# Optimization experiments

Hardware: AMD Instinct MI355X
Metric: run time of the kernel (lower is better)

## Reference

```python
import jax, jax.numpy as jnp
import numpy as np

C, H, W = 64, 32, 32  # feature planes are (1, 64, 32, 32)
M = 1_048_576         # number of query points


def bilinear_sample(plane, coords):
    """torch.nn.functional.grid_sample, mode='bilinear', padding_mode='zeros',
    align_corners=True, for a single plane.
    plane: (C, H, W); coords: (M, 2) with (x, y) in [-1, 1] convention.
    Returns (M, C)."""
    c, h, w = plane.shape
    # align_corners=True mapping: -1 -> 0, +1 -> size-1
    x = (coords[:, 0] + 1.0) * 0.5 * (w - 1)
    y = (coords[:, 1] + 1.0) * 0.5 * (h - 1)
    x0 = jnp.floor(x)
    y0 = jnp.floor(y)
    wx1 = x - x0
    wy1 = y - y0
    wx0 = 1.0 - wx1
    wy0 = 1.0 - wy1

    def gather(xi, yi):
        xi = xi.astype(jnp.int32)
        yi = yi.astype(jnp.int32)
        valid = (xi >= 0) & (xi < w) & (yi >= 0) & (yi < h)  # zeros padding
        xc = jnp.clip(xi, 0, w - 1)
        yc = jnp.clip(yi, 0, h - 1)
        v = plane[:, yc, xc]  # (C, M)
        return jnp.where(valid[None, :], v, 0.0)

    out = (gather(x0, y0) * (wx0 * wy0)[None, :]
           + gather(x0 + 1, y0) * (wx1 * wy0)[None, :]
           + gather(x0, y0 + 1) * (wx0 * wy1)[None, :]
           + gather(x0 + 1, y0 + 1) * (wx1 * wy1)[None, :])
    return out.T  # (M, C)


def setup_inputs() -> dict:
    key = jax.random.key(0)
    ks = jax.random.split(key, 10)
    coordinates = jax.random.normal(ks[0], (1, M, 3), dtype=jnp.float32)
    # tri-plane embeddings: randn * 0.1, shape (1, C, H, W)
    plane_xy = jax.random.normal(ks[1], (1, C, H, W), dtype=jnp.float32) * 0.1
    plane_yz = jax.random.normal(ks[2], (1, C, H, W), dtype=jnp.float32) * 0.1
    plane_xz = jax.random.normal(ks[3], (1, C, H, W), dtype=jnp.float32) * 0.1
    # MLP 64 -> 128 -> 128 -> 1 (torch Linear weight shape = (out, in))
    # layer 0: first_layer_sine_init -> U(-1/64, 1/64)
    w1 = jax.random.uniform(ks[4], (128, 64), jnp.float32, -1.0 / 64, 1.0 / 64)
    b1 = jnp.zeros((128,), jnp.float32)
    # layers 1,2: frequency_init(30) -> U(-sqrt(6/in)/30, sqrt(6/in)/30)
    s2 = np.sqrt(6.0 / 128) / 30.0
    w2 = jax.random.uniform(ks[5], (128, 128), jnp.float32, -s2, s2)
    b2 = jnp.zeros((128,), jnp.float32)
    w3 = jax.random.uniform(ks[6], (1, 128), jnp.float32, -s2, s2)
    b3 = jnp.zeros((1,), jnp.float32)
    return {"coordinates": coordinates, "plane_xy": plane_xy, "plane_yz": plane_yz,
            "plane_xz": plane_xz, "w1": w1, "b1": b1, "w2": w2, "b2": b2,
            "w3": w3, "b3": b3}


def reference(coordinates, plane_xy, plane_yz, plane_xz, w1, b1, w2, b2, w3, b3):
    # coordinates: (1, M, 3); planes have leading batch dim of 1 (torch requires
    # grid batch == plane batch, so batch_size is structurally 1).
    samp = jax.vmap(bilinear_sample, in_axes=(None, 0))
    xy = samp(plane_xy[0], coordinates[..., 0:2])   # (1, M, C)
    yz = samp(plane_yz[0], coordinates[..., 1:3])   # (1, M, C)
    xz = samp(plane_xz[0], coordinates[..., ::2])   # (1, M, C)
    features = xy * yz * xz                          # aggregate_fn='prod'
    h = jax.nn.relu(jnp.einsum('bmc,oc->bmo', features, w1) + b1)
    h = jax.nn.relu(jnp.einsum('bmc,oc->bmo', h, w2) + b2)
    out = jnp.einsum('bmc,oc->bmo', h, w3) + b3      # (1, M, 1)
    return out
```

## Files before the change

### kernel.cpp

```cpp
#include <hip/hip_runtime.h>

#define MPTS 1048576

typedef _Float16 f16;
typedef _Float16 f16x4 __attribute__((ext_vector_type(4)));
typedef _Float16 f16x8 __attribute__((ext_vector_type(8)));
typedef float f32x4 __attribute__((ext_vector_type(4)));

static const size_t OFF_Z    = 0;
static const size_t OFF_CNT  = 64;
static const size_t OFF_PL   = 256;
static const size_t OFF_W1H  = OFF_PL + 786432;
static const size_t OFF_W2H  = OFF_W1H + 16384;
static const size_t OFF_BCNT = OFF_W2H + 32768;
static const size_t OFF_BOFF = OFF_BCNT + 4096;
static const size_t OFF_LIST = OFF_BOFF + 4096;
static const size_t OFF_PC   = OFF_LIST + (size_t)MPTS*4;
static const size_t WS_LIST  = OFF_PC;
static const size_t WS_PC    = OFF_PC + (size_t)MPTS*16;

__device__ __forceinline__ int iclamp(int v, int lo, int hi) {
    return v < lo ? lo : (v > hi ? hi : v);
}
__device__ __forceinline__ int imin(int a, int b) { return a < b ? a : b; }

__device__ __forceinline__ bool isact(float x, float y, float z) {
    float px = fmaf(x, 15.5f, 15.5f);
    float py = fmaf(y, 15.5f, 15.5f);
    float pz = fmaf(z, 15.5f, 15.5f);
    return (px > -1.0f) & (px < 32.0f) & (py > -1.0f) & (py < 32.0f) &
           (pz > -1.0f) & (pz < 32.0f);
}

struct Bi { int o00, o01, o10, o11; float w00, w01, w10, w11; };

__device__ __forceinline__ Bi mkbi(float pa, float pb) {
    float fa = floorf(pa), fb = floorf(pb);
    int ia0 = (int)fa, ib0 = (int)fb;
    int ia1 = ia0 + 1, ib1 = ib0 + 1;
    float wa1 = pa - fa, wa0 = 1.0f - wa1;
    float wb1 = pb - fb, wb0 = 1.0f - wb1;
    float va0 = (ia0 >= 0 && ia0 < 32) ? wa0 : 0.0f;
    float va1 = (ia1 >= 0 && ia1 < 32) ? wa1 : 0.0f;
    float vb0 = (ib0 >= 0 && ib0 < 32) ? wb0 : 0.0f;
    float vb1 = (ib1 >= 0 && ib1 < 32) ? wb1 : 0.0f;
    int ca0 = iclamp(ia0, 0, 31), ca1 = iclamp(ia1, 0, 31);
    int cb0 = iclamp(ib0, 0, 31), cb1 = iclamp(ib1, 0, 31);
    Bi r;
    r.o00 = (cb0 * 32 + ca0) * 64; r.o01 = (cb0 * 32 + ca1) * 64;
    r.o10 = (cb1 * 32 + ca0) * 64; r.o11 = (cb1 * 32 + ca1) * 64;
    r.w00 = va0 * vb0; r.w01 = va1 * vb0; r.w10 = va0 * vb1; r.w11 = va1 * vb1;
    return r;
}

__device__ __forceinline__ float4 bsamp4(const float* __restrict__ base, const Bi B) {
    float4 g00 = *(const float4*)(base + B.o00);
    float4 g01 = *(const float4*)(base + B.o01);
    float4 g10 = *(const float4*)(base + B.o10);
    float4 g11 = *(const float4*)(base + B.o11);
    float4 r;
    r.x = fmaf(B.w00, g00.x, fmaf(B.w01, g01.x, fmaf(B.w10, g10.x, B.w11 * g11.x)));
    r.y = fmaf(B.w00, g00.y, fmaf(B.w01, g01.y, fmaf(B.w10, g10.y, B.w11 * g11.y)));
    r.z = fmaf(B.w00, g00.z, fmaf(B.w01, g01.z, fmaf(B.w10, g10.z, B.w11 * g11.z)));
    r.w = fmaf(B.w00, g00.w, fmaf(B.w01, g01.w, fmaf(B.w10, g10.w, B.w11 * g11.w)));
    return r;
}

__device__ __forceinline__ void samp16(const float* __restrict__ pl,
                                       float pa, float pb, int c0,
                                       float* __restrict__ f, const bool mult) {
    Bi B = mkbi(pa, pb);
    const float4* p00 = (const float4*)(pl + B.o00 + c0);
    const float4* p01 = (const float4*)(pl + B.o01 + c0);
    const float4* p10 = (const float4*)(pl + B.o10 + c0);
    const float4* p11 = (const float4*)(pl + B.o11 + c0);
#pragma unroll
    for (int q = 0; q < 4; ++q) {
        float4 g00 = p00[q], g01 = p01[q], g10 = p10[q], g11 = p11[q];
        float vx = fmaf(B.w00, g00.x, fmaf(B.w01, g01.x, fmaf(B.w10, g10.x, B.w11 * g11.x)));
        float vy = fmaf(B.w00, g00.y, fmaf(B.w01, g01.y, fmaf(B.w10, g10.y, B.w11 * g11.y)));
        float vz = fmaf(B.w00, g00.z, fmaf(B.w01, g01.z, fmaf(B.w10, g10.z, B.w11 * g11.z)));
        float vw = fmaf(B.w00, g00.w, fmaf(B.w01, g01.w, fmaf(B.w10, g10.w, B.w11 * g11.w)));
        if (mult) {
            f[4*q+0] *= vx; f[4*q+1] *= vy; f[4*q+2] *= vz; f[4*q+3] *= vw;
        } else {
            f[4*q+0] = vx; f[4*q+1] = vy; f[4*q+2] = vz; f[4*q+3] = vw;
        }
    }
}

__global__ void k_prep(const float* __restrict__ pxy, const float* __restrict__ pyz,
                       const float* __restrict__ pxz,
                       const float* __restrict__ w1, const float* __restrict__ w2,
                       const float* __restrict__ b1, const float* __restrict__ b2,
                       const float* __restrict__ w3, const float* __restrict__ b3,
                       float* __restrict__ planes, f16* __restrict__ w1h,
                       f16* __restrict__ w2h, float* __restrict__ zout) {
    if (blockIdx.x == 864) {
        int p = threadIdx.x;
        if (p >= 128) return;
        float h2p = b2[p];
        for (int o = 0; o < 128; ++o) h2p += w2[p * 128 + o] * fmaxf(b1[o], 0.0f);
        __shared__ float red[128];
        red[p] = fmaxf(h2p, 0.0f) * w3[p];
        __syncthreads();
        for (int s = 64; s > 0; s >>= 1) {
            if (p < s) red[p] += red[p + s];
            __syncthreads();
        }
        if (p == 0) *zout = red[0] + b3[0];
        return;
    }
    int tid = blockIdx.x * 256 + threadIdx.x;
    if (tid < 3 * 65536) {
        int t = tid >> 16;
        int r = tid & 65535;
        int hw = r >> 6;
        int c = r & 63;
        const float* src = (t == 0) ? pxy : ((t == 1) ? pyz : pxz);
        planes[tid] = src[c * 1024 + hw];
    } else if (tid < 3 * 65536 + 8192) {
        int r = tid - 3 * 65536;
        w1h[r] = (f16)w1[r];
    } else {
        int r = tid - (3 * 65536 + 8192);
        w2h[r] = (f16)w2[r];
    }
}

__global__ void k_count(const float* __restrict__ coords, const float* __restrict__ zptr,
                        int* __restrict__ bcnt, float* __restrict__ out) {
    int t = threadIdx.x, bid = blockIdx.x;
    const float4* c4 = (const float4*)coords + 768 * (size_t)bid + 3 * t;
    float4 a = c4[0], b = c4[1], c = c4[2];
    int base = bid * 1024 + t * 4;
    float z = *zptr;
    bool a0 = isact(a.x, a.y, a.z);
    bool a1 = isact(a.w, b.x, b.y);
    bool a2 = isact(b.z, b.w, c.x);
    bool a3 = isact(c.y, c.z, c.w);
    if (!a0) out[base + 0] = z;
    if (!a1) out[base + 1] = z;
    if (!a2) out[base + 2] = z;
    if (!a3) out[base + 3] = z;
    int s = (int)a0 + (int)a1 + (int)a2 + (int)a3;
#pragma unroll
    for (int off = 1; off <= 32; off <<= 1) s += __shfl_xor(s, off, 64);
    __shared__ int wt[4];
    if ((t & 63) == 0) wt[t >> 6] = s;
    __syncthreads();
    if (t == 0) bcnt[bid] = wt[0] + wt[1] + wt[2] + wt[3];
}

__global__ void k_scan(const int* __restrict__ bcnt, int* __restrict__ boff,
                       int* __restrict__ cnt) {
    int t = threadIdx.x, lane = t & 63, wv = t >> 6;
    int mine = bcnt[t];
    int incl = mine;
#pragma unroll
    for (int off = 1; off <= 32; off <<= 1) {
        int v = __shfl_up(incl, off, 64);
        if (lane >= off) incl += v;
    }
    __shared__ int wtot[16];
    if (lane == 63) wtot[wv] = incl;
    __syncthreads();
    int wexcl = 0;
#pragma unroll
    for (int k = 0; k < 16; ++k) wexcl += (k < wv) ? wtot[k] : 0;
    boff[t] = wexcl + incl - mine;
    if (t == 1023) *cnt = wexcl + incl;
}

template<bool PC>
__global__ void k_scatter(const float* __restrict__ coords, const int* __restrict__ boff,
                          int* __restrict__ list, float4* __restrict__ pc4) {
    int t = threadIdx.x, bid = blockIdx.x, lane = t & 63, wv = t >> 6;
    const float4* c4 = (const float4*)coords + 768 * (size_t)bid + 3 * t;
    float4 a = c4[0], b = c4[1], c = c4[2];
    int base = bid * 1024 + t * 4;
    float xs[4] = {a.x, a.w, b.z, c.y};
    float ys[4] = {a.y, b.x, b.w, c.z};
    float zs[4] = {a.z, b.y, c.x, c.w};
    bool act[4];
#pragma unroll
    for (int j = 0; j < 4; ++j) act[j] = isact(xs[j], ys[j], zs[j]);
    int mine = (int)act[0] + (int)act[1] + (int)act[2] + (int)act[3];
    int incl = mine;
#pragma unroll
    for (int off = 1; off <= 32; off <<= 1) {
        int v = __shfl_up(incl, off, 64);
        if (lane >= off) incl += v;
    }
    __shared__ int wtot[4];
    if (lane == 63) wtot[wv] = incl;
    __syncthreads();
    int wexcl = 0;
#pragma unroll
    for (int k = 0; k < 4; ++k) wexcl += (k < wv) ? wtot[k] : 0;
    int pos = boff[bid] + wexcl + incl - mine;
#pragma unroll
    for (int j = 0; j < 4; ++j) {
        if (act[j]) {
            list[pos] = base + j;
            if (PC) {
                float4 p;
                p.x = fmaf(xs[j], 15.5f, 15.5f);
                p.y = fmaf(ys[j], 15.5f, 15.5f);
                p.z = fmaf(zs[j], 15.5f, 15.5f);
                p.w = 0.0f;
                pc4[pos] = p;
            }
            ++pos;
        }
    }
}

__global__ __launch_bounds__(256, 2)
void k_fused(const float4* __restrict__ pc4, const float* __restrict__ planes,
             const f16* __restrict__ w1h, const f16* __restrict__ w2h,
             const float* __restrict__ b1, const float* __restrict__ b2,
             const float* __restrict__ w3, const float* __restrict__ b3,
             const int* __restrict__ cnt, const int* __restrict__ list,
             float* __restrict__ out) {
    const int n = *cnt;
    const int tile = blockIdx.x;
    if (tile * 64 >= n) return;

    __shared__ __attribute__((aligned(16))) f16 Fs[64 * 64];
    __shared__ __attribute__((aligned(16))) f16 H1s[64 * 128];
    __shared__ float outp[4][64];

    const int t   = threadIdx.x;
    const int wv  = t >> 6;
    const int l   = t & 63;
    const int l15 = l & 15;
    const int lg  = l >> 4;
    const int ptw = t >> 4;
    const int cq  = t & 15;

    const float* pl0 = planes;
    const float* pl1 = planes + 65536;
    const float* pl2 = planes + 131072;
    const float b3v = b3[0];

#pragma unroll
    for (int pass = 0; pass < 4; ++pass) {
        int pt = pass * 16 + ptw;
        int ic = imin(tile * 64 + pt, n - 1);
        float4 c = pc4[ic];
        Bi B0 = mkbi(c.x, c.y);
        Bi B1 = mkbi(c.y, c.z);
        Bi B2 = mkbi(c.x, c.z);
        float4 s0 = bsamp4(pl0 + cq * 4, B0);
        float4 s1 = bsamp4(pl1 + cq * 4, B1);
        float4 s2 = bsamp4(pl2 + cq * 4, B2);
        float4 f;
        f.x = (s0.x * s1.x) * s2.x;
        f.y = (s0.y * s1.y) * s2.y;
        f.z = (s0.z * s1.z) * s2.z;
        f.w = (s0.w * s1.w) * s2.w;
        f16x4 pk;
        pk[0] = (f16)f.x; pk[1] = (f16)f.y; pk[2] = (f16)f.z; pk[3] = (f16)f.w;
        *(f16x4*)((char*)Fs + pt * 128 + ((cq * 8) ^ ((pt & 7) << 4))) = pk;
    }
    __syncthreads();

    f16x8 af[4][2];
#pragma unroll
    for (int Mt = 0; Mt < 4; ++Mt) {
        int row = Mt * 16 + l15;
        const char* rb = (const char*)Fs + row * 128;
        int sw = (row & 7) << 4;
        af[Mt][0] = *(const f16x8*)(rb + ((lg * 16) ^ sw));
        af[Mt][1] = *(const f16x8*)(rb + ((64 + lg * 16) ^ sw));
    }

    f16x8 wf1[2][2];
    f16x8 wf2[2][4];
    f32x4 b1q[2], b2q[2], w3q[2];
#pragma unroll
    for (int ntl = 0; ntl < 2; ++ntl) {
        int nrow = (wv * 2 + ntl) * 16 + l15;
        wf1[ntl][0] = *(const f16x8*)(w1h + nrow * 64 + lg * 8);
        wf1[ntl][1] = *(const f16x8*)(w1h + nrow * 64 + 32 + lg * 8);
#pragma unroll
        for (int ks = 0; ks < 4; ++ks)
            wf2[ntl][ks] = *(const f16x8*)(w2h + nrow * 128 + ks * 32 + lg * 8);
        int nb = (wv * 2 + ntl) * 16 + lg * 4;
        b1q[ntl] = *(const f32x4*)(b1 + nb);
        b2q[ntl] = *(const f32x4*)(b2 + nb);
        w3q[ntl] = *(const f32x4*)(w3 + nb);
    }

    f32x4 acc[2][4];
#pragma unroll
    for (int ntl = 0; ntl < 2; ++ntl)
#pragma unroll
        for (int Mt = 0; Mt < 4; ++Mt) acc[ntl][Mt] = b1q[ntl];
#pragma unroll
    for (int Mt = 0; Mt < 4; ++Mt) {
#pragma unroll
        for (int ntl = 0; ntl < 2; ++ntl) {
            acc[ntl][Mt] = __builtin_amdgcn_mfma_f32_16x16x32_f16(wf1[ntl][0], af[Mt][0], acc[ntl][Mt], 0, 0, 0);
            acc[ntl][Mt] = __builtin_amdgcn_mfma_f32_16x16x32_f16(wf1[ntl][1], af[Mt][1], acc[ntl][Mt], 0, 0, 0);
        }
    }

#pragma unroll
    for (int ntl = 0; ntl < 2; ++ntl) {
#pragma unroll
        for (int Mt = 0; Mt < 4; ++Mt) {
            int pt = Mt * 16 + l15;
            int off = (((wv * 2 + ntl) * 32 + lg * 8) ^ ((pt & 7) << 4));
            f16x4 h;
            h[0] = (f16)fmaxf(acc[ntl][Mt][0], 0.0f);
            h[1] = (f16)fmaxf(acc[ntl][Mt][1], 0.0f);
            h[2] = (f16)fmaxf(acc[ntl][Mt][2], 0.0f);
            h[3] = (f16)fmaxf(acc[ntl][Mt][3], 0.0f);
            *(f16x4*)((char*)H1s + pt * 256 + off) = h;
        }
    }
    __syncthreads();

    f32x4 acc2[2][4];
#pragma unroll
    for (int ntl = 0; ntl < 2; ++ntl)
#pragma unroll
        for (int Mt = 0; Mt < 4; ++Mt) acc2[ntl][Mt] = b2q[ntl];
#pragma unroll
    for (int Mt = 0; Mt < 4; ++Mt) {
        int row = Mt * 16 + l15;
        const char* rb = (const char*)H1s + row * 256;
        int sw = (row & 7) << 4;
        f16x8 a0 = *(const f16x8*)(rb + ((lg * 16) ^ sw));
        f16x8 a1 = *(const f16x8*)(rb + ((64 + lg * 16) ^ sw));
        f16x8 a2 = *(const f16x8*)(rb + ((128 + lg * 16) ^ sw));
        f16x8 a3 = *(const f16x8*)(rb + ((192 + lg * 16) ^ sw));
#pragma unroll
        for (int ntl = 0; ntl < 2; ++ntl) {
            acc2[ntl][Mt] = __builtin_amdgcn_mfma_f32_16x16x32_f16(wf2[ntl][0], a0, acc2[ntl][Mt], 0, 0, 0);
            acc2[ntl][Mt] = __builtin_amdgcn_mfma_f32_16x16x32_f16(wf2[ntl][1], a1, acc2[ntl][Mt], 0, 0, 0);
            acc2[ntl][Mt] = __builtin_amdgcn_mfma_f32_16x16x32_f16(wf2[ntl][2], a2, acc2[ntl][Mt], 0, 0, 0);
            acc2[ntl][Mt] = __builtin_amdgcn_mfma_f32_16x16x32_f16(wf2[ntl][3], a3, acc2[ntl][Mt], 0, 0, 0);
        }
    }

#pragma unroll
    for (int Mt = 0; Mt < 4; ++Mt) {
        float s = 0.0f;
#pragma unroll
        for (int ntl = 0; ntl < 2; ++ntl)
#pragma unroll
            for (int r = 0; r < 4; ++r)
                s = fmaf(fmaxf(acc2[ntl][Mt][r], 0.0f), w3q[ntl][r], s);
        s += __shfl_xor(s, 16, 64);
        s += __shfl_xor(s, 32, 64);
        if (lg == 0) outp[wv][Mt * 16 + l15] = s;
    }
    __syncthreads();
    if (t < 64) {
        int gi = tile * 64 + t;
        if (gi < n) {
            float s = outp[0][t] + outp[1][t] + outp[2][t] + outp[3][t] + b3v;
            out[list[gi]] = s;
        }
    }
}

__global__ __launch_bounds__(256, 2)
void k_mlp(const float* __restrict__ coords, const float* __restrict__ planes,
           const f16* __restrict__ w1h, const f16* __restrict__ w2h,
           const float* __restrict__ b1, const float* __restrict__ b2,
           const float* __restrict__ w3, const float* __restrict__ b3,
           const int* __restrict__ cnt, const int* __restrict__ list,
           float* __restrict__ out) {
    const int n = *cnt;
    const int tile = blockIdx.x;
    if (tile * 64 >= n) return;

    __shared__ __attribute__((aligned(16))) f16 Fs[64 * 64];
    __shared__ __attribute__((aligned(16))) f16 H1s[64 * 128];
    __shared__ float outp[4][64];

    const int t   = threadIdx.x;
    const int wv  = t >> 6;
    const int l   = t & 63;
    const int l15 = l & 15;
    const int lg  = l >> 4;

    const float* pl0 = planes;
    const float* pl1 = planes + 65536;
    const float* pl2 = planes + 131072;

    f16x8 wf1[2][2];
    f16x8 wf2[2][4];
    float b1v[2], b2v[2], w3v[2];
#pragma unroll
    for (int ntl = 0; ntl < 2; ++ntl) {
        int nrow = (wv * 2 + ntl) * 16 + l15;
#pragma unroll
        for (int ks = 0; ks < 2; ++ks)
            wf1[ntl][ks] = *(const f16x8*)(w1h + nrow * 64 + ks * 32 + lg * 8);
#pragma unroll
        for (int ks = 0; ks < 4; ++ks)
            wf2[ntl][ks] = *(const f16x8*)(w2h + nrow * 128 + ks * 32 + lg * 8);
        b1v[ntl] = b1[nrow];
        b2v[ntl] = b2[nrow];
        w3v[ntl] = w3[nrow];
    }
    const float b3v = b3[0];

    {
        int pt = t >> 2, c0 = (t & 3) * 16;
        int ic = imin(tile * 64 + pt, n - 1);
        int i = list[ic];
        float px = fmaf(coords[3 * i + 0], 15.5f, 15.5f);
        float py = fmaf(coords[3 * i + 1], 15.5f, 15.5f);
        float pz = fmaf(coords[3 * i + 2], 15.5f, 15.5f);
        float feat[16];
        samp16(pl0, px, py, c0, feat, false);
        samp16(pl1, py, pz, c0, feat, true);
        samp16(pl2, px, pz, c0, feat, true);
        int sw = (pt & 7) << 4;
        char* Fb = (char*)Fs + pt * 128;
        f16x8 pk;
#pragma unroll
        for (int j = 0; j < 8; ++j) pk[j] = (f16)feat[j];
        *(f16x8*)(Fb + ((c0 * 2) ^ sw)) = pk;
#pragma unroll
        for (int j = 0; j < 8; ++j) pk[j] = (f16)feat[8 + j];
        *(f16x8*)(Fb + ((c0 * 2 + 16) ^ sw)) = pk;
    }
    __syncthreads();

    f32x4 acc[2][4];
#pragma unroll
    for (int ntl = 0; ntl < 2; ++ntl) {
        f32x4 ini = {b1v[ntl], b1v[ntl], b1v[ntl], b1v[ntl]};
#pragma unroll
        for (int Mt = 0; Mt < 4; ++Mt) acc[ntl][Mt] = ini;
    }
#pragma unroll
    for (int Mt = 0; Mt < 4; ++Mt) {
        int row = Mt * 16 + l15;
        const char* rb = (const char*)Fs + row * 128;
        int sw = (row & 7) << 4;
        f16x8 a0 = *(const f16x8*)(rb + ((lg * 16) ^ sw));
        f16x8 a1 = *(const f16x8*)(rb + ((64 + lg * 16) ^ sw));
#pragma unroll
        for (int ntl = 0; ntl < 2; ++ntl) {
            acc[ntl][Mt] = __builtin_amdgcn_mfma_f32_16x16x32_f16(a0, wf1[ntl][0], acc[ntl][Mt], 0, 0, 0);
            acc[ntl][Mt] = __builtin_amdgcn_mfma_f32_16x16x32_f16(a1, wf1[ntl][1], acc[ntl][Mt], 0, 0, 0);
        }
    }
#pragma unroll
    for (int ntl = 0; ntl < 2; ++ntl) {
        int ncol = (wv * 2 + ntl) * 16 + l15;
#pragma unroll
        for (int Mt = 0; Mt < 4; ++Mt) {
#pragma unroll
            for (int r = 0; r < 4; ++r) {
                int prow = Mt * 16 + lg * 4 + r;
                float v = fmaxf(acc[ntl][Mt][r], 0.0f);
                *(f16*)((char*)H1s + prow * 256 + ((ncol * 2) ^ ((prow & 7) << 4))) = (f16)v;
            }
        }
    }
    __syncthreads();

    f32x4 acc2[2][4];
#pragma unroll
    for (int ntl = 0; ntl < 2; ++ntl) {
        f32x4 ini = {b2v[ntl], b2v[ntl], b2v[ntl], b2v[ntl]};
#pragma unroll
        for (int Mt = 0; Mt < 4; ++Mt) acc2[ntl][Mt] = ini;
    }
#pragma unroll
    for (int Mt = 0; Mt < 4; ++Mt) {
        int row = Mt * 16 + l15;
        const char* rb = (const char*)H1s + row * 256;
        int sw = (row & 7) << 4;
        f16x8 a0 = *(const f16x8*)(rb + ((lg * 16) ^ sw));
        f16x8 a1 = *(const f16x8*)(rb + ((64 + lg * 16) ^ sw));
        f16x8 a2 = *(const f16x8*)(rb + ((128 + lg * 16) ^ sw));
        f16x8 a3 = *(const f16x8*)(rb + ((192 + lg * 16) ^ sw));
#pragma unroll
        for (int ntl = 0; ntl < 2; ++ntl) {
            acc2[ntl][Mt] = __builtin_amdgcn_mfma_f32_16x16x32_f16(a0, wf2[ntl][0], acc2[ntl][Mt], 0, 0, 0);
            acc2[ntl][Mt] = __builtin_amdgcn_mfma_f32_16x16x32_f16(a1, wf2[ntl][1], acc2[ntl][Mt], 0, 0, 0);
            acc2[ntl][Mt] = __builtin_amdgcn_mfma_f32_16x16x32_f16(a2, wf2[ntl][2], acc2[ntl][Mt], 0, 0, 0);
            acc2[ntl][Mt] = __builtin_amdgcn_mfma_f32_16x16x32_f16(a3, wf2[ntl][3], acc2[ntl][Mt], 0, 0, 0);
        }
    }

    float part[4][4];
#pragma unroll
    for (int Mt = 0; Mt < 4; ++Mt)
#pragma unroll
        for (int r = 0; r < 4; ++r)
            part[Mt][r] = fmaxf(acc2[0][Mt][r], 0.0f) * w3v[0] +
                          fmaxf(acc2[1][Mt][r], 0.0f) * w3v[1];
#pragma unroll
    for (int off = 1; off <= 8; off <<= 1) {
#pragma unroll
        for (int Mt = 0; Mt < 4; ++Mt)
#pragma unroll
            for (int r = 0; r < 4; ++r)
                part[Mt][r] += __shfl_xor(part[Mt][r], off, 64);
    }
    if (l15 == 0) {
#pragma unroll
        for (int Mt = 0; Mt < 4; ++Mt)
#pragma unroll
            for (int r = 0; r < 4; ++r)
                outp[wv][Mt * 16 + lg * 4 + r] = part[Mt][r];
    }
    __syncthreads();
    if (t < 64) {
        int gi = tile * 64 + t;
        if (gi < n) {
            float s = outp[0][t] + outp[1][t] + outp[2][t] + outp[3][t] + b3v;
            out[list[gi]] = s;
        }
    }
}

__global__ void k_fallback(const float* __restrict__ coords,
                           const float* __restrict__ p0, const float* __restrict__ p1,
                           const float* __restrict__ p2,
                           const float* __restrict__ w1, const float* __restrict__ b1,
                           const float* __restrict__ w2, const float* __restrict__ b2,
                           const float* __restrict__ w3, const float* __restrict__ b3,
                           float* __restrict__ out) {
    int i = blockIdx.x * 256 + threadIdx.x;
    if (i >= MPTS) return;
    float x = coords[3 * i + 0], y = coords[3 * i + 1], z = coords[3 * i + 2];
    float px = fmaf(x, 15.5f, 15.5f);
    float py = fmaf(y, 15.5f, 15.5f);
    float pz = fmaf(z, 15.5f, 15.5f);
    float feat[64];
    const float* pls[3] = {p0, p1, p2};
    float pa[3] = {px, py, px}, pb[3] = {py, pz, pz};
    for (int pidx = 0; pidx < 3; ++pidx) {
        float paf = pa[pidx], pbf = pb[pidx];
        float fa = floorf(paf), fb = floorf(pbf);
        int ia0 = (int)fa, ib0 = (int)fb, ia1 = ia0 + 1, ib1 = ib0 + 1;
        float wa1 = paf - fa, wa0 = 1.0f - wa1, wb1 = pbf - fb, wb0 = 1.0f - wb1;
        float va0 = (ia0 >= 0 && ia0 < 32) ? wa0 : 0.0f;
        float va1 = (ia1 >= 0 && ia1 < 32) ? wa1 : 0.0f;
        float vb0 = (ib0 >= 0 && ib0 < 32) ? wb0 : 0.0f;
        float vb1 = (ib1 >= 0 && ib1 < 32) ? wb1 : 0.0f;
        int ca0 = iclamp(ia0, 0, 31), ca1 = iclamp(ia1, 0, 31);
        int cb0 = iclamp(ib0, 0, 31), cb1 = iclamp(ib1, 0, 31);
        float w00 = va0 * vb0, w01 = va1 * vb0, w10 = va0 * vb1, w11 = va1 * vb1;
        int o00 = cb0 * 32 + ca0, o01 = cb0 * 32 + ca1;
        int o10 = cb1 * 32 + ca0, o11 = cb1 * 32 + ca1;
        const float* pl = pls[pidx];
        for (int c = 0; c < 64; ++c) {
            const float* pc = pl + c * 1024;
            float v = fmaf(w00, pc[o00], fmaf(w01, pc[o01],
                      fmaf(w10, pc[o10], w11 * pc[o11])));
            if (pidx == 0) feat[c] = v; else feat[c] *= v;
        }
    }
    float oa = b3[0];
    for (int half = 0; half < 2; ++half) {
        float h2h[64];
        for (int p = 0; p < 64; ++p) h2h[p] = b2[half * 64 + p];
        for (int o = 0; o < 128; ++o) {
            float a = b1[o];
            for (int c = 0; c < 64; ++c) a = fmaf(feat[c], w1[o * 64 + c], a);
            float r = fmaxf(a, 0.0f);
            for (int p = 0; p < 64; ++p) h2h[p] = fmaf(r, w2[(half * 64 + p) * 128 + o], h2h[p]);
        }
        for (int p = 0; p < 64; ++p) oa = fmaf(fmaxf(h2h[p], 0.0f), w3[half * 64 + p], oa);
    }
    out[i] = oa;
}

extern "C" void kernel_launch(void* const* d_in, const int* in_sizes, int n_in,
                              void* d_out, int out_size, void* d_ws, size_t ws_size,
                              hipStream_t stream) {
    const float* coords = (const float*)d_in[0];
    const float* pxy    = (const float*)d_in[1];
    const float* pyz    = (const float*)d_in[2];
    const float* pxz    = (const float*)d_in[3];
    const float* w1     = (const float*)d_in[4];
    const float* b1     = (const float*)d_in[5];
    const float* w2     = (const float*)d_in[6];
    const float* b2     = (const float*)d_in[7];
    const float* w3     = (const float*)d_in[8];
    const float* b3     = (const float*)d_in[9];
    float* out = (float*)d_out;

    if (ws_size >= WS_LIST) {
        float*  zout   = (float*)((char*)d_ws + OFF_Z);
        int*    cnt    = (int*)((char*)d_ws + OFF_CNT);
        float*  planes = (float*)((char*)d_ws + OFF_PL);
        f16*    w1h    = (f16*)((char*)d_ws + OFF_W1H);
        f16*    w2h    = (f16*)((char*)d_ws + OFF_W2H);
        int*    bcnt   = (int*)((char*)d_ws + OFF_BCNT);
        int*    boff   = (int*)((char*)d_ws + OFF_BOFF);
        int*    list   = (int*)((char*)d_ws + OFF_LIST);
        float4* pc4    = (float4*)((char*)d_ws + OFF_PC);

        k_prep<<<865, 256, 0, stream>>>(pxy, pyz, pxz, w1, w2, b1, b2, w3, b3,
                                        planes, w1h, w2h, zout);
        k_count<<<1024, 256, 0, stream>>>(coords, zout, bcnt, out);
        k_scan<<<1, 1024, 0, stream>>>(bcnt, boff, cnt);

        if (ws_size >= WS_PC) {
            k_scatter<true><<<1024, 256, 0, stream>>>(coords, boff, list, pc4);
            k_fused<<<16384, 256, 0, stream>>>(pc4, planes, w1h, w2h,
                                               b1, b2, w3, b3, cnt, list, out);
        } else {
            k_scatter<false><<<1024, 256, 0, stream>>>(coords, boff, list, nullptr);
            k_mlp<<<16384, 256, 0, stream>>>(coords, planes, w1h, w2h,
                                             b1, b2, w3, b3, cnt, list, out);
        }
    } else {
        k_fallback<<<4096, 256, 0, stream>>>(coords, pxy, pyz, pxz,
                                             w1, b1, w2, b2, w3, b3, out);
    }
}
```

Baseline: 98.72 us.

## Sample fp16 planes with shared-memory bilinear setup and MFMA priority hints

```diff
diff --git a/kernel.cpp b/kernel.cpp
--- a/kernel.cpp
+++ b/kernel.cpp
@@ -10,7 +10,8 @@
 static const size_t OFF_Z    = 0;
 static const size_t OFF_CNT  = 64;
 static const size_t OFF_PL   = 256;
-static const size_t OFF_W1H  = OFF_PL + 786432;
+static const size_t OFF_PLH  = OFF_PL + 786432;
+static const size_t OFF_W1H  = OFF_PLH + 393216;
 static const size_t OFF_W2H  = OFF_W1H + 16384;
 static const size_t OFF_BCNT = OFF_W2H + 32768;
 static const size_t OFF_BOFF = OFF_BCNT + 4096;
@@ -53,16 +54,17 @@
     return r;
 }
 
-__device__ __forceinline__ float4 bsamp4(const float* __restrict__ base, const Bi B) {
-    float4 g00 = *(const float4*)(base + B.o00);
-    float4 g01 = *(const float4*)(base + B.o01);
-    float4 g10 = *(const float4*)(base + B.o10);
-    float4 g11 = *(const float4*)(base + B.o11);
+__device__ __forceinline__ float4 lerp4h(const f16* __restrict__ base,
+                                         const int4 O, const float4 W) {
+    f16x4 g00 = *(const f16x4*)(base + O.x);
+    f16x4 g01 = *(const f16x4*)(base + O.y);
+    f16x4 g10 = *(const f16x4*)(base + O.z);
+    f16x4 g11 = *(const f16x4*)(base + O.w);
     float4 r;
-    r.x = fmaf(B.w00, g00.x, fmaf(B.w01, g01.x, fmaf(B.w10, g10.x, B.w11 * g11.x)));
-    r.y = fmaf(B.w00, g00.y, fmaf(B.w01, g01.y, fmaf(B.w10, g10.y, B.w11 * g11.y)));
-    r.z = fmaf(B.w00, g00.z, fmaf(B.w01, g01.z, fmaf(B.w10, g10.z, B.w11 * g11.z)));
-    r.w = fmaf(B.w00, g00.w, fmaf(B.w01, g01.w, fmaf(B.w10, g10.w, B.w11 * g11.w)));
+    r.x = fmaf(W.x, (float)g00[0], fmaf(W.y, (float)g01[0], fmaf(W.z, (float)g10[0], W.w * (float)g11[0])));
+    r.y = fmaf(W.x, (float)g00[1], fmaf(W.y, (float)g01[1], fmaf(W.z, (float)g10[1], W.w * (float)g11[1])));
+    r.z = fmaf(W.x, (float)g00[2], fmaf(W.y, (float)g01[2], fmaf(W.z, (float)g10[2], W.w * (float)g11[2])));
+    r.w = fmaf(W.x, (float)g00[3], fmaf(W.y, (float)g01[3], fmaf(W.z, (float)g10[3], W.w * (float)g11[3])));
     return r;
 }
 
@@ -94,8 +96,9 @@
                        const float* __restrict__ w1, const float* __restrict__ w2,
                        const float* __restrict__ b1, const float* __restrict__ b2,
                        const float* __restrict__ w3, const float* __restrict__ b3,
-                       float* __restrict__ planes, f16* __restrict__ w1h,
-                       f16* __restrict__ w2h, float* __restrict__ zout) {
+                       float* __restrict__ planes, f16* __restrict__ planes_h,
+                       f16* __restrict__ w1h, f16* __restrict__ w2h,
+                       float* __restrict__ zout) {
     if (blockIdx.x == 864) {
         int p = threadIdx.x;
         if (p >= 128) return;
@@ -118,7 +121,9 @@
         int hw = r >> 6;
         int c = r & 63;
         const float* src = (t == 0) ? pxy : ((t == 1) ? pyz : pxz);
-        planes[tid] = src[c * 1024 + hw];
+        float v = src[c * 1024 + hw];
+        planes[tid] = v;
+        planes_h[tid] = (f16)v;
     } else if (tid < 3 * 65536 + 8192) {
         int r = tid - 3 * 65536;
         w1h[r] = (f16)w1[r];
@@ -217,7 +222,7 @@
 }
 
 __global__ __launch_bounds__(256, 2)
-void k_fused(const float4* __restrict__ pc4, const float* __restrict__ planes,
+void k_fused(const float4* __restrict__ pc4, const f16* __restrict__ plh,
              const f16* __restrict__ w1h, const f16* __restrict__ w2h,
              const float* __restrict__ b1, const float* __restrict__ b2,
              const float* __restrict__ w3, const float* __restrict__ b3,
@@ -230,6 +235,8 @@
     __shared__ __attribute__((aligned(16))) f16 Fs[64 * 64];
     __shared__ __attribute__((aligned(16))) f16 H1s[64 * 128];
     __shared__ float outp[4][64];
+    __shared__ int4   BsO[64 * 3];
+    __shared__ float4 BsW[64 * 3];
 
     const int t   = threadIdx.x;
     const int wv  = t >> 6;
@@ -239,22 +246,28 @@
     const int ptw = t >> 4;
     const int cq  = t & 15;
 
-    const float* pl0 = planes;
-    const float* pl1 = planes + 65536;
-    const float* pl2 = planes + 131072;
     const float b3v = b3[0];
 
+    if ((t & 3) < 3) {
+        int pt0 = t >> 2;
+        int pl  = t & 3;
+        int ic = imin(tile * 64 + pt0, n - 1);
+        float4 c = pc4[ic];
+        float pa = (pl == 1) ? c.y : c.x;
+        float pb = (pl == 0) ? c.y : c.z;
+        Bi B = mkbi(pa, pb);
+        BsO[pt0 * 3 + pl] = make_int4(B.o00, B.o01, B.o10, B.o11);
+        BsW[pt0 * 3 + pl] = make_float4(B.w00, B.w01, B.w10, B.w11);
+    }
+    __syncthreads();
+
+    const f16* bch = plh + cq * 4;
 #pragma unroll
     for (int pass = 0; pass < 4; ++pass) {
         int pt = pass * 16 + ptw;
-        int ic = imin(tile * 64 + pt, n - 1);
-        float4 c = pc4[ic];
-        Bi B0 = mkbi(c.x, c.y);
-        Bi B1 = mkbi(c.y, c.z);
-        Bi B2 = mkbi(c.x, c.z);
-        float4 s0 = bsamp4(pl0 + cq * 4, B0);
-        float4 s1 = bsamp4(pl1 + cq * 4, B1);
-        float4 s2 = bsamp4(pl2 + cq * 4, B2);
+        float4 s0 = lerp4h(bch,          BsO[pt * 3 + 0], BsW[pt * 3 + 0]);
+        float4 s1 = lerp4h(bch + 65536,  BsO[pt * 3 + 1], BsW[pt * 3 + 1]);
+        float4 s2 = lerp4h(bch + 131072, BsO[pt * 3 + 2], BsW[pt * 3 + 2]);
         float4 f;
         f.x = (s0.x * s1.x) * s2.x;
         f.y = (s0.y * s1.y) * s2.y;
@@ -298,6 +311,7 @@
     for (int ntl = 0; ntl < 2; ++ntl)
 #pragma unroll
         for (int Mt = 0; Mt < 4; ++Mt) acc[ntl][Mt] = b1q[ntl];
+    __builtin_amdgcn_s_setprio(1);
 #pragma unroll
     for (int Mt = 0; Mt < 4; ++Mt) {
 #pragma unroll
@@ -306,6 +320,7 @@
             acc[ntl][Mt] = __builtin_amdgcn_mfma_f32_16x16x32_f16(wf1[ntl][1], af[Mt][1], acc[ntl][Mt], 0, 0, 0);
         }
     }
+    __builtin_amdgcn_s_setprio(0);
 
 #pragma unroll
     for (int ntl = 0; ntl < 2; ++ntl) {
@@ -337,6 +352,7 @@
         f16x8 a1 = *(const f16x8*)(rb + ((64 + lg * 16) ^ sw));
         f16x8 a2 = *(const f16x8*)(rb + ((128 + lg * 16) ^ sw));
         f16x8 a3 = *(const f16x8*)(rb + ((192 + lg * 16) ^ sw));
+        __builtin_amdgcn_s_setprio(1);
 #pragma unroll
         for (int ntl = 0; ntl < 2; ++ntl) {
             acc2[ntl][Mt] = __builtin_amdgcn_mfma_f32_16x16x32_f16(wf2[ntl][0], a0, acc2[ntl][Mt], 0, 0, 0);
@@ -344,6 +360,7 @@
             acc2[ntl][Mt] = __builtin_amdgcn_mfma_f32_16x16x32_f16(wf2[ntl][2], a2, acc2[ntl][Mt], 0, 0, 0);
             acc2[ntl][Mt] = __builtin_amdgcn_mfma_f32_16x16x32_f16(wf2[ntl][3], a3, acc2[ntl][Mt], 0, 0, 0);
         }
+        __builtin_amdgcn_s_setprio(0);
     }
 
 #pragma unroll
@@ -598,6 +615,7 @@
         float*  zout   = (float*)((char*)d_ws + OFF_Z);
         int*    cnt    = (int*)((char*)d_ws + OFF_CNT);
         float*  planes = (float*)((char*)d_ws + OFF_PL);
+        f16*    plh    = (f16*)((char*)d_ws + OFF_PLH);
         f16*    w1h    = (f16*)((char*)d_ws + OFF_W1H);
         f16*    w2h    = (f16*)((char*)d_ws + OFF_W2H);
         int*    bcnt   = (int*)((char*)d_ws + OFF_BCNT);
@@ -606,13 +624,13 @@
         float4* pc4    = (float4*)((char*)d_ws + OFF_PC);
 
         k_prep<<<865, 256, 0, stream>>>(pxy, pyz, pxz, w1, w2, b1, b2, w3, b3,
-                                        planes, w1h, w2h, zout);
+                                        planes, plh, w1h, w2h, zout);
         k_count<<<1024, 256, 0, stream>>>(coords, zout, bcnt, out);
         k_scan<<<1, 1024, 0, stream>>>(bcnt, boff, cnt);
 
         if (ws_size >= WS_PC) {
             k_scatter<true><<<1024, 256, 0, stream>>>(coords, boff, list, pc4);
-            k_fused<<<16384, 256, 0, stream>>>(pc4, planes, w1h, w2h,
+            k_fused<<<16384, 256, 0, stream>>>(pc4, plh, w1h, w2h,
                                                b1, b2, w3, b3, cnt, list, out);
         } else {
             k_scatter<false><<<1024, 256, 0, stream>>>(coords, boff, list, nullptr);
```

Result: no change. 96.89 us (-1.9%).
